# Optimization experiments

Hardware: AMD Instinct MI355X
Metric: run time of the kernel (lower is better)

Reference implementation:

```python
import jax, jax.numpy as jnp
import numpy as np

B, N, C = 4, 4096, 512
H = 8          # num_heads
M = 64         # num_landmarks
HD = C // H    # head_dim = 64
N_ITER = 6     # Newton-Schulz iterations (Nystromformer default)


def iterative_inv(mat):
    # mat: [B, H, M, M]; Nystromformer pseudo-inverse via Newton-Schulz.
    I = jnp.eye(mat.shape[-1], dtype=mat.dtype)
    K = mat
    # global-max initialization (original Nystromformer 'original' init)
    V = K.swapaxes(-1, -2) / (jnp.max(jnp.sum(K, axis=-2)) * jnp.max(jnp.sum(K, axis=-1)))
    for _ in range(N_ITER):
        KV = jnp.matmul(K, V)
        V = 0.25 * jnp.matmul(V, 13.0 * I - jnp.matmul(KV, 15.0 * I - jnp.matmul(KV, 7.0 * I - KV)))
    return V


def setup_inputs() -> dict:
    key = jax.random.key(0)
    k1, k2, k3, k4 = jax.random.split(key, 4)
    s = C ** -0.5
    return {
        "x": jax.random.normal(k1, (B, N, C), dtype=jnp.float32),
        "qkv_w": jax.random.normal(k2, (3 * C, C), dtype=jnp.float32) * s,
        "proj_w": jax.random.normal(k3, (C, C), dtype=jnp.float32) * s,
        "proj_b": jax.random.normal(k4, (C,), dtype=jnp.float32) * 0.01,
        "epoch": 1,
    }


def reference(x, qkv_w, proj_w, proj_b, epoch):
    b, n, c = x.shape
    hd = c // H
    qkv = (x @ qkv_w.T).reshape(b, n, 3, H, hd).transpose(2, 0, 3, 1, 4)  # [3,B,H,N,hd]
    Q, K, V = qkv[0], qkv[1], qkv[2]
    scale = 1.0 / np.sqrt(np.sqrt(hd)).astype(np.float32)
    Q = Q * scale
    K = K * scale
    # landmark pooling: mean over segments of length N // M
    Ql = Q.reshape(b, H, M, n // M, hd).mean(axis=-2)  # [B,H,M,hd]
    Kl = K.reshape(b, H, M, n // M, hd).mean(axis=-2)
    kernel_1 = jax.nn.softmax(jnp.einsum('bhnd,bhmd->bhnm', Q, Kl), axis=-1)   # [B,H,N,M]
    kernel_2 = jax.nn.softmax(jnp.einsum('bhmd,bhld->bhml', Ql, Kl), axis=-1)  # [B,H,M,M]
    kernel_3 = jax.nn.softmax(jnp.einsum('bhmd,bhnd->bhmn', Ql, K), axis=-1)   # [B,H,M,N]
    X = jnp.matmul(jnp.matmul(kernel_1, iterative_inv(kernel_2)), jnp.matmul(kernel_3, V))
    X = X.transpose(0, 2, 1, 3).reshape(b, n, c)
    return X @ proj_w.T + proj_b
```

## Files before the change

kernel.cpp:

```cpp
#include <hip/hip_runtime.h>
#include <hip/hip_bf16.h>
#include <stdint.h>

#define QSZe 8388608ull

typedef __attribute__((ext_vector_type(8))) short bf16x8;
typedef __attribute__((ext_vector_type(4))) float f32x4;
typedef const __attribute__((address_space(1))) unsigned int* gas1_t;
typedef __attribute__((address_space(3))) unsigned int* las3_t;

__device__ __forceinline__ float bf2f(unsigned short u) {
  return __uint_as_float(((unsigned int)u) << 16);
}
__device__ __forceinline__ unsigned short f2bf(float f) {
  unsigned int u = __float_as_uint(f);
  unsigned int r = (u + 0x7FFFu + ((u >> 16) & 1u)) >> 16;
  return (unsigned short)r;
}
__device__ __forceinline__ void gload_lds16(const void* g, void* l) {
  __builtin_amdgcn_global_load_lds((gas1_t)g, (las3_t)l, 16, 0, 0);
}
__device__ __forceinline__ unsigned int detect_f32(
    const unsigned short* __restrict__ raw_x) {
  int lane = threadIdx.x & 63;
  int big = 0;
#pragma unroll
  for (int i = 0; i < 4; i++) {
    int e = (raw_x[lane * 4 + i] >> 7) & 0xFF;
    big |= (e >= 0x8F) ? 1 : 0;
  }
  return (__ballot(big) != 0ull) ? 1u : 0u;
}

__global__ __launch_bounds__(256) void conv_all(
    const void* __restrict__ rx, const void* __restrict__ rwq,
    const void* __restrict__ rwp, unsigned short* __restrict__ cx,
    unsigned short* __restrict__ cwq, unsigned short* __restrict__ cwp,
    unsigned int* __restrict__ gstat) {
  int gid = blockIdx.x * 256 + threadIdx.x;
  if (gid == 0) {
    gstat[0] = 0u;
    gstat[1] = 0u;
  }
  unsigned int f = detect_f32((const unsigned short*)rx);
  const void* src;
  unsigned short* dst;
  int i8;
  if (gid < 1048576) {
    if (!f) return;
    src = rx; dst = cx; i8 = gid * 8;
  } else if (gid < 1146880) {
    src = rwq; dst = cwq; i8 = (gid - 1048576) * 8;
  } else {
    src = rwp; dst = cwp; i8 = (gid - 1146880) * 8;
  }
  if (f) {
    const float* fp = (const float*)src;
    float4 a = *(const float4*)(fp + i8);
    float4 b = *(const float4*)(fp + i8 + 4);
    unsigned short o[8] = {f2bf(a.x), f2bf(a.y), f2bf(a.z), f2bf(a.w),
                           f2bf(b.x), f2bf(b.y), f2bf(b.z), f2bf(b.w)};
    *(uint4*)(dst + i8) = *(const uint4*)o;
  } else {
    *(uint4*)(dst + i8) = *(const uint4*)((const unsigned short*)src + i8);
  }
}

__device__ __forceinline__ void mmB(const unsigned short* A_R,
                                    const unsigned short* B_T,
                                    unsigned short* out_R,
                                    unsigned short* out_T, int wave, int lane,
                                    float s, float dg, float a7,
                                    const unsigned short* Aelt) {
  const int fr = lane & 15, fq = lane >> 4;
  bf16x8 af0 = *(const bf16x8*)&A_R[(wave * 16 + fr) * 64 + fq * 8];
  bf16x8 af1 = *(const bf16x8*)&A_R[(wave * 16 + fr) * 64 + 32 + fq * 8];
  f32x4 acc[4] = {};
#pragma unroll
  for (int j = 0; j < 4; j++) {
    bf16x8 b0 = *(const bf16x8*)&B_T[(j * 16 + fr) * 64 + fq * 8];
    bf16x8 b1 = *(const bf16x8*)&B_T[(j * 16 + fr) * 64 + 32 + fq * 8];
    acc[j] = __builtin_amdgcn_mfma_f32_16x16x32_bf16(af0, b0, acc[j], 0, 0, 0);
    acc[j] = __builtin_amdgcn_mfma_f32_16x16x32_bf16(af1, b1, acc[j], 0, 0, 0);
  }
  float ael[4][4];
  if (Aelt) {
#pragma unroll
    for (int j = 0; j < 4; j++)
#pragma unroll
      for (int r = 0; r < 4; r++)
        ael[j][r] = bf2f(Aelt[(wave * 16 + fq * 4 + r) * 64 + j * 16 + fr]);
  }
#pragma unroll
  for (int j = 0; j < 4; j++) {
    int col = j * 16 + fr;
    unsigned short pack[4];
#pragma unroll
    for (int r = 0; r < 4; r++) {
      int row = wave * 16 + fq * 4 + r;
      float v = s * acc[j][r] + ((row == col) ? dg : 0.0f);
      if (Aelt) v += a7 * ael[j][r];
      unsigned short bv = f2bf(v);
      if (out_R) out_R[row * 64 + col] = bv;
      pack[r] = bv;
    }
    if (out_T)
      *(uint2*)&out_T[col * 64 + wave * 16 + fq * 4] = *(const uint2*)pack;
  }
}

__global__ __launch_bounds__(512) void qkv_gemm_mfma(
    const unsigned short* __restrict__ w, const void* __restrict__ xraw,
    const unsigned short* __restrict__ cx, unsigned short* __restrict__ qkv,
    float* __restrict__ Ql, float* __restrict__ Kl,
    unsigned short* __restrict__ Qlb, unsigned short* __restrict__ Klb) {
  __shared__ __align__(16) unsigned short At[2][128 * 64];
  __shared__ __align__(16) unsigned short Bt[2][256 * 64];
  const int t = threadIdx.x;
  const int lane = t & 63, wave = t >> 6;
  const int wf = wave >> 2, wt = wave & 3;
  const unsigned int isf = detect_f32((const unsigned short*)xraw);
  const unsigned short* xb = isf ? cx : (const unsigned short*)xraw;
  const int lin = blockIdx.x + blockIdx.y * 12;
  const int swz = (lin & 7) * 96 + (lin >> 3);
  const int f0 = (swz % 12) * 128, n0g = (swz / 12) * 256;
  const int srow = lane >> 3, skc = ((lane & 7) ^ srow) * 8;
  const int fr = lane & 15, fq = lane >> 4;
  const int rsw = fr & 7;
  f32x4 acc[4][4] = {};

  auto STAGE = [&](int p, int k0) {
#pragma unroll
    for (int s = 0; s < 2; s++) {
      int inst = wave * 2 + s;
      int row = inst * 8 + srow;
      gload_lds16(w + (size_t)(f0 + row) * 512 + k0 + skc,
                  &At[p][inst * 512]);
    }
#pragma unroll
    for (int s = 0; s < 4; s++) {
      int inst = wave * 4 + s;
      int row = inst * 8 + srow;
      gload_lds16(xb + (size_t)(n0g + row) * 512 + k0 + skc,
                  &Bt[p][inst * 512]);
    }
  };
  auto COMPUTE = [&](int p) {
#pragma unroll
    for (int kk = 0; kk < 64; kk += 32) {
      const int swo = (((kk >> 3) + fq) ^ rsw) << 3;
      bf16x8 af[4], bxf[4];
#pragma unroll
      for (int i = 0; i < 4; i++)
        af[i] = *(const bf16x8*)&At[p][(wf * 64 + i * 16 + fr) * 64 + swo];
#pragma unroll
      for (int j = 0; j < 4; j++)
        bxf[j] = *(const bf16x8*)&Bt[p][(wt * 64 + j * 16 + fr) * 64 + swo];
#pragma unroll
      for (int i = 0; i < 4; i++)
#pragma unroll
        for (int j = 0; j < 4; j++)
          acc[i][j] = __builtin_amdgcn_mfma_f32_16x16x32_bf16(
              af[i], bxf[j], acc[i][j], 0, 0, 0);
    }
  };

  STAGE(0, 0);
  int p = 0;
#pragma unroll 1
  for (int k0 = 0; k0 < 512; k0 += 64) {
    if (k0 + 64 < 512) {
      STAGE(p ^ 1, k0 + 64);
      asm volatile("s_waitcnt vmcnt(6)" ::: "memory");
    } else {
      asm volatile("s_waitcnt vmcnt(0)" ::: "memory");
    }
    asm volatile("s_barrier" ::: "memory");
    COMPUTE(p);
    asm volatile("s_barrier" ::: "memory");
    p ^= 1;
  }
  const int fbase = f0 + wf * 64;
  const int which = fbase >> 9;
  const int h = (fbase >> 6) & 7;
  const float scale = (which < 2) ? 0.3535533905932738f : 1.0f;
  const int b_ = n0g >> 12;
  const int bh = b_ * 8 + h;
  const int m_loc = ((n0g + wt * 64) & 4095) >> 6;
#pragma unroll
  for (int i = 0; i < 4; i++) {
    int d0 = i * 16 + fq * 4;
#pragma unroll
    for (int j = 0; j < 4; j++) {
      int nn = (n0g + wt * 64 + j * 16 + fr) & 4095;
      unsigned short pack[4];
#pragma unroll
      for (int r = 0; r < 4; r++) pack[r] = f2bf(acc[i][j][r] * scale);
      *(uint2*)&qkv[(size_t)which * QSZe + ((size_t)bh * 4096 + nn) * 64 +
                    d0] = *(const uint2*)pack;
    }
  }
  if (which < 2) {
    const float ps = scale * (1.0f / 64.0f);
#pragma unroll
    for (int i = 0; i < 4; i++) {
      float sm[4];
#pragma unroll
      for (int r = 0; r < 4; r++)
        sm[r] = acc[i][0][r] + acc[i][1][r] + acc[i][2][r] + acc[i][3][r];
#pragma unroll
      for (int mask = 1; mask < 16; mask <<= 1)
#pragma unroll
        for (int r = 0; r < 4; r++) sm[r] += __shfl_xor(sm[r], mask, 64);
      if (fr == 0) {
        int d0 = i * 16 + fq * 4;
        float4 v4 = make_float4(sm[0] * ps, sm[1] * ps, sm[2] * ps, sm[3] * ps);
        unsigned short pk[4] = {f2bf(v4.x), f2bf(v4.y), f2bf(v4.z), f2bf(v4.w)};
        size_t off = (size_t)bh * 4096 + m_loc * 64 + d0;
        if (which == 0) {
          *(float4*)&Ql[off] = v4;
          *(uint2*)&Qlb[off] = *(const uint2*)pk;
        } else {
          *(float4*)&Kl[off] = v4;
          *(uint2*)&Klb[off] = *(const uint2*)pk;
        }
      }
    }
  }
}

__global__ __launch_bounds__(256) void k3k2_mfma(
    const unsigned short* __restrict__ Qlb,
    const unsigned short* __restrict__ qkv, float* __restrict__ Wp,
    float* __restrict__ sp, const float* __restrict__ Ql,
    const float* __restrict__ Kl, float* __restrict__ k2,
    unsigned int* __restrict__ gstat) {
  __shared__ __align__(16) unsigned char SM[35840];
  const int t = threadIdx.x;
  const int lane = t & 63, wave = t >> 6;
  const int slab = blockIdx.x, bh = blockIdx.y;

  if (slab == 8) {
    float* KlT = (float*)SM;
    float* Ps = (float*)(SM + 16384);
#pragma unroll
    for (int i = 0; i < 16; i++) {
      int idx = i * 256 + t;
      KlT[(idx & 63) * 64 + (idx >> 6)] = Kl[bh * 4096 + idx];
    }
    __syncthreads();
    for (int r = wave * 16; r < wave * 16 + 16; r++) {
      float qv = Ql[(bh * 64 + r) * 64 + lane];
      float acc = 0.f;
#pragma unroll
      for (int k = 0; k < 64; k++)
        acc += __shfl(qv, k, 64) * KlT[k * 64 + lane];
      float mx = acc;
#pragma unroll
      for (int o = 32; o > 0; o >>= 1) mx = fmaxf(mx, __shfl_xor(mx, o, 64));
      float e = __expf(acc - mx);
      float s = e;
#pragma unroll
      for (int o = 32; o > 0; o >>= 1) s += __shfl_xor(s, o, 64);
      float p = e / s;
      k2[(bh * 64 + r) * 64 + lane] = p;
      Ps[r * 65 + lane] = p;
    }
    __syncthreads();
    float val = 0.f;
    if (t < 64) {
      for (int r = 0; r < 64; r++) val += Ps[r * 65 + t];
    } else if (t < 128) {
      int r = t - 64;
      for (int c = 0; c < 64; c++) val += Ps[r * 65 + c];
    }
    float mv = val;
#pragma unroll
    for (int o = 32; o > 0; o >>= 1) mv = fmaxf(mv, __shfl_xor(mv, o, 64));
    if (t == 0) atomicMax(gstat + 0, __float_as_uint(mv));
    if (t == 64) atomicMax(gstat + 1, __float_as_uint(mv));
    return;
  }
  unsigned short* Et = (unsigned short*)SM;
  unsigned short* Vt = (unsigned short*)(SM + 17408);
  float* scol_l = (float*)(SM + 34816);
  const int fr = lane & 15, fq = lane >> 4;
  const int n_base = slab * 512;
  const unsigned short* Kb = qkv + QSZe + (size_t)bh * 262144;
  const unsigned short* Vb = qkv + 2 * QSZe + (size_t)bh * 262144;
  const unsigned short* Qlp = Qlb + bh * 4096;

  bf16x8 qb[2][4];
#pragma unroll
  for (int h = 0; h < 2; h++)
#pragma unroll
    for (int j = 0; j < 4; j++)
      qb[h][j] = *(const bf16x8*)(Qlp + (j * 16 + fr) * 64 + h * 32 + fq * 8);

  f32x4 accW[4] = {};
  float scol[4] = {0.f, 0.f, 0.f, 0.f};

  for (int sc = 0; sc < 4; sc++) {
    const int n0 = n_base + sc * 128;
    {
      int n = t & 127, dg = t >> 7;
#pragma unroll
      for (int i = 0; i < 4; i++) {
        int d0 = (dg + 2 * i) * 8;
        uint4 v = *(const uint4*)(Vb + (size_t)(n0 + n) * 64 + d0);
        const unsigned short* s = (const unsigned short*)&v;
#pragma unroll
        for (int u = 0; u < 8; u++) Vt[(d0 + u) * 136 + n] = s[u];
      }
    }
    f32x4 acc[2][4] = {};
#pragma unroll
    for (int i = 0; i < 2; i++) {
      const unsigned short* Kr =
          Kb + (size_t)(n0 + wave * 32 + i * 16 + fr) * 64;
      bf16x8 a0 = *(const bf16x8*)(Kr + fq * 8);
      bf16x8 a1 = *(const bf16x8*)(Kr + 32 + fq * 8);
#pragma unroll
      for (int j = 0; j < 4; j++) {
        acc[i][j] = __builtin_amdgcn_mfma_f32_16x16x32_bf16(a0, qb[0][j],
                                                            acc[i][j], 0, 0, 0);
        acc[i][j] = __builtin_amdgcn_mfma_f32_16x16x32_bf16(a1, qb[1][j],
                                                            acc[i][j], 0, 0, 0);
      }
    }
#pragma unroll
    for (int i = 0; i < 2; i++)
#pragma unroll
      for (int j = 0; j < 4; j++) {
        unsigned short pack[4];
        float s4 = 0.f;
#pragma unroll
        for (int r = 0; r < 4; r++) {
          float e = __expf(acc[i][j][r]);
          s4 += e;
          pack[r] = f2bf(e);
        }
        scol[j] += s4;
        *(uint2*)&Et[(j * 16 + fr) * 136 + wave * 32 + i * 16 + fq * 4] =
            *(const uint2*)pack;
      }
    __syncthreads();
#pragma unroll
    for (int kk = 0; kk < 128; kk += 32) {
      bf16x8 ap = *(const bf16x8*)&Et[(wave * 16 + fr) * 136 + kk + fq * 8];
#pragma unroll
      for (int j = 0; j < 4; j++) {
        bf16x8 bv = *(const bf16x8*)&Vt[(j * 16 + fr) * 136 + kk + fq * 8];
        accW[j] =
            __builtin_amdgcn_mfma_f32_16x16x32_bf16(ap, bv, accW[j], 0, 0, 0);
      }
    }
    __syncthreads();
  }
#pragma unroll
  for (int j = 0; j < 4; j++) {
    float s = scol[j];
    s += __shfl_xor(s, 16, 64);
    s += __shfl_xor(s, 32, 64);
    if (fq == 0) scol_l[wave * 64 + j * 16 + fr] = s;
  }
  __syncthreads();
  if (t < 64)
    sp[(bh * 8 + slab) * 64 + t] = scol_l[0 * 64 + t] + scol_l[1 * 64 + t] +
                                   scol_l[2 * 64 + t] + scol_l[3 * 64 + t];
  float* wpo = Wp + ((size_t)bh * 8 + slab) * 4096;
#pragma unroll
  for (int j = 0; j < 4; j++)
#pragma unroll
    for (int r = 0; r < 4; r++)
      wpo[(wave * 16 + fq * 4 + r) * 64 + j * 16 + fr] = accW[j][r];
}

__global__ __launch_bounds__(256) void ns_kernel(
    const float* __restrict__ k2g, const unsigned int* __restrict__ gstat,
    const float* __restrict__ Wp, const float* __restrict__ sp,
    unsigned short* __restrict__ Ztb) {
  __shared__ __align__(16) unsigned short L[8 * 4096];
  __shared__ float ssum[64];
  unsigned short* K2R = L;
  unsigned short* VR = L + 4096;
  unsigned short* VT = L + 2 * 4096;
  unsigned short* AR = L + 3 * 4096;
  unsigned short* AT = L + 4 * 4096;
  unsigned short* T2T = L + 5 * 4096;
  unsigned short* T3T = L + 6 * 4096;
  unsigned short* WT = L + 7 * 4096;
  const int t = threadIdx.x, bh = blockIdx.x;
  const int lane = t & 63, wave = t >> 6;
  const float scale =
      1.0f / (__uint_as_float(gstat[0]) * __uint_as_float(gstat[1]));
  const float* k2p = k2g + bh * 4096;
  if (t < 64) {
    float s = 0.f;
#pragma unroll
    for (int c = 0; c < 8; c++) s += sp[(bh * 8 + c) * 64 + t];
    ssum[t] = s;
  }
  __syncthreads();
#pragma unroll
  for (int i = 0; i < 16; i++) {
    int idx = i * 256 + t;
    int m = idx >> 6, d = idx & 63;
    float kv = k2p[idx];
    K2R[idx] = f2bf(kv);
    VT[idx] = f2bf(kv * scale);
    VR[idx] = f2bf(k2p[d * 64 + m] * scale);
    float wv = 0.f;
#pragma unroll
    for (int cc = 0; cc < 8; cc++)
      wv += Wp[((size_t)(bh * 8 + cc)) * 4096 + idx];
    WT[d * 64 + m] = f2bf(wv / ssum[m]);
  }
  __syncthreads();
  for (int it = 0; it < 6; it++) {
    mmB(K2R, VT, AR, AT, wave, lane, 1.0f, 0.0f, 0.0f, nullptr);
    __syncthreads();
    mmB(AR, AT, nullptr, T2T, wave, lane, 1.0f, 15.0f, -7.0f, AR);
    __syncthreads();
    mmB(AR, T2T, nullptr, T3T, wave, lane, -1.0f, 13.0f, 0.0f, nullptr);
    __syncthreads();
    mmB(VR, T3T, VR, VT, wave, lane, 0.25f, 0.0f, 0.0f, nullptr);
    __syncthreads();
  }
  {
    const int fr = lane & 15, fq = lane >> 4;
    bf16x8 af0 = *(const bf16x8*)&WT[(wave * 16 + fr) * 64 + fq * 8];
    bf16x8 af1 = *(const bf16x8*)&WT[(wave * 16 + fr) * 64 + 32 + fq * 8];
    f32x4 acc[4] = {};
#pragma unroll
    for (int j = 0; j < 4; j++) {
      bf16x8 b0 = *(const bf16x8*)&VR[(j * 16 + fr) * 64 + fq * 8];
      bf16x8 b1 = *(const bf16x8*)&VR[(j * 16 + fr) * 64 + 32 + fq * 8];
      acc[j] =
          __builtin_amdgcn_mfma_f32_16x16x32_bf16(af0, b0, acc[j], 0, 0, 0);
      acc[j] =
          __builtin_amdgcn_mfma_f32_16x16x32_bf16(af1, b1, acc[j], 0, 0, 0);
    }
#pragma unroll
    for (int j = 0; j < 4; j++) {
      int m = j * 16 + fr;
#pragma unroll
      for (int r = 0; r < 4; r++) {
        int d = wave * 16 + fq * 4 + r;
        Ztb[bh * 4096 + d * 64 + m] = f2bf(acc[j][r]);
      }
    }
  }
}

__global__ __launch_bounds__(256) void k1x_mfma(
    const unsigned short* __restrict__ qkv,
    const unsigned short* __restrict__ Klb,
    const unsigned short* __restrict__ Ztb, unsigned short* __restrict__ X) {
  __shared__ __align__(16) unsigned short Qt[128 * 64];
  __shared__ __align__(16) unsigned short Ps[128 * 72];
  const int t = threadIdx.x;
  const int lane = t & 63, wave = t >> 6;
  const int fr = lane & 15, fq = lane >> 4;
  const int rsw = fr & 7;
  const int bh = blockIdx.x;
  const int n0 = blockIdx.y * 128;
  const unsigned short* Qb = qkv + (size_t)bh * 262144 + (size_t)n0 * 64;
  const unsigned short* Klp = Klb + bh * 4096;
  const unsigned short* Ztp = Ztb + bh * 4096;

  {
    const int srow = lane >> 3, skc = ((lane & 7) ^ srow) * 8;
#pragma unroll
    for (int s = 0; s < 4; s++) {
      int inst = wave * 4 + s;
      gload_lds16(Qb + (size_t)(inst * 8 + srow) * 64 + skc, &Qt[inst * 512]);
    }
  }
  __syncthreads();

  f32x4 acc[2][4] = {};
#pragma unroll
  for (int kk = 0; kk < 64; kk += 32) {
    bf16x8 af[2], bg[4];
#pragma unroll
    for (int i = 0; i < 2; i++)
      af[i] = *(const bf16x8*)&Qt[(wave * 32 + i * 16 + fr) * 64 +
                                  ((((kk >> 3) + fq) ^ rsw) << 3)];
#pragma unroll
    for (int j = 0; j < 4; j++)
      bg[j] = *(const bf16x8*)(Klp + (j * 16 + fr) * 64 + kk + fq * 8);
#pragma unroll
    for (int i = 0; i < 2; i++)
#pragma unroll
      for (int j = 0; j < 4; j++)
        acc[i][j] = __builtin_amdgcn_mfma_f32_16x16x32_bf16(af[i], bg[j],
                                                            acc[i][j], 0, 0, 0);
  }

#pragma unroll
  for (int i = 0; i < 2; i++) {
    float sr[4] = {0.f, 0.f, 0.f, 0.f};
#pragma unroll
    for (int j = 0; j < 4; j++)
#pragma unroll
      for (int r = 0; r < 4; r++) {
        float e = __expf(acc[i][j][r]);
        acc[i][j][r] = e;
        sr[r] += e;
      }
#pragma unroll
    for (int mask = 1; mask < 16; mask <<= 1)
#pragma unroll
      for (int r = 0; r < 4; r++) sr[r] += __shfl_xor(sr[r], mask, 64);
    float is[4];
#pragma unroll
    for (int r = 0; r < 4; r++) is[r] = 1.0f / sr[r];
#pragma unroll
    for (int j = 0; j < 4; j++)
#pragma unroll
      for (int r = 0; r < 4; r++)
        Ps[(wave * 32 + i * 16 + fq * 4 + r) * 72 + j * 16 + fr] =
            f2bf(acc[i][j][r] * is[r]);
  }
  __syncthreads();

  f32x4 ax[2][4] = {};
#pragma unroll
  for (int kk = 0; kk < 64; kk += 32) {
    bf16x8 ap[2], bz[4];
#pragma unroll
    for (int i = 0; i < 2; i++)
      ap[i] =
          *(const bf16x8*)&Ps[(wave * 32 + i * 16 + fr) * 72 + kk + fq * 8];
#pragma unroll
    for (int j = 0; j < 4; j++)
      bz[j] = *(const bf16x8*)(Ztp + (j * 16 + fr) * 64 + kk + fq * 8);
#pragma unroll
    for (int i = 0; i < 2; i++)
#pragma unroll
      for (int j = 0; j < 4; j++)
        ax[i][j] = __builtin_amdgcn_mfma_f32_16x16x32_bf16(ap[i], bz[j],
                                                           ax[i][j], 0, 0, 0);
  }

  const int b_ = bh >> 3, h = bh & 7;
#pragma unroll
  for (int i = 0; i < 2; i++) {
#pragma unroll
    for (int j = 0; j < 4; j++) {
      int c = h * 64 + j * 16 + fr;
#pragma unroll
      for (int r = 0; r < 4; r++) {
        int n = n0 + wave * 32 + i * 16 + fq * 4 + r;
        X[((size_t)(b_ * 4096 + n)) * 512 + c] = f2bf(ax[i][j][r]);
      }
    }
  }
}

__global__ __launch_bounds__(256) void proj_gemm_mfma(
    const unsigned short* __restrict__ X, const unsigned short* __restrict__ w,
    const unsigned short* __restrict__ raw_x, const void* __restrict__ raw_b,
    float* __restrict__ out) {
  __shared__ __align__(16) unsigned short At[128 * 64];
  __shared__ __align__(16) unsigned short Bt[128 * 64];
  const int t = threadIdx.x;
  const unsigned int f = detect_f32(raw_x);
  const int lane = t & 63, wave = t >> 6;
  const int wr = wave >> 1, wc = wave & 1;
  const int i0 = blockIdx.y * 128, j0 = blockIdx.x * 128;
  const int srow = lane >> 3;
  const int skc = ((lane & 7) ^ srow) * 8;
  const int fr = lane & 15, fq = lane >> 4;
  const int rsw = fr & 7;
  f32x4 acc[4][4] = {};

  for (int k0 = 0; k0 < 512; k0 += 64) {
#pragma unroll
    for (int s = 0; s < 4; s++) {
      int inst = wave * 4 + s;
      int row = inst * 8 + srow;
      gload_lds16(X + (size_t)(i0 + row) * 512 + k0 + skc, &At[inst * 512]);
      gload_lds16(w + (size_t)(j0 + row) * 512 + k0 + skc, &Bt[inst * 512]);
    }
    __syncthreads();
#pragma unroll
    for (int kk = 0; kk < 64; kk += 32) {
      const int swo = (((kk >> 3) + fq) ^ rsw) << 3;
      bf16x8 af[4], bg[4];
#pragma unroll
      for (int i = 0; i < 4; i++)
        af[i] = *(const bf16x8*)&At[(wr * 64 + i * 16 + fr) * 64 + swo];
#pragma unroll
      for (int j = 0; j < 4; j++)
        bg[j] = *(const bf16x8*)&Bt[(wc * 64 + j * 16 + fr) * 64 + swo];
#pragma unroll
      for (int i = 0; i < 4; i++)
#pragma unroll
        for (int j = 0; j < 4; j++)
          acc[i][j] = __builtin_amdgcn_mfma_f32_16x16x32_bf16(
              af[i], bg[j], acc[i][j], 0, 0, 0);
    }
    __syncthreads();
  }
#pragma unroll
  for (int j = 0; j < 4; j++) {
    int col = j0 + wc * 64 + j * 16 + fr;
    float bia = f ? ((const float*)raw_b)[col]
                  : bf2f(((const unsigned short*)raw_b)[col]);
#pragma unroll
    for (int i = 0; i < 4; i++) {
      int rbase = i0 + wr * 64 + i * 16 + fq * 4;
#pragma unroll
      for (int r = 0; r < 4; r++) {
        out[(size_t)(rbase + r) * 512 + col] = acc[i][j][r] + bia;
      }
    }
  }
}

extern "C" void kernel_launch(void* const* d_in, const int* in_sizes, int n_in,
                              void* d_out, int out_size, void* d_ws,
                              size_t ws_size, hipStream_t stream) {
  (void)in_sizes; (void)n_in; (void)out_size; (void)ws_size;

  char* w8 = (char*)d_ws;
  unsigned short* cx  = (unsigned short*)(w8 + 0);
  unsigned short* cwq = (unsigned short*)(w8 + 16777216);
  unsigned short* cwp = (unsigned short*)(w8 + 18350080);
  unsigned short* qkv = (unsigned short*)(w8 + 18876416);
  unsigned short* X   = (unsigned short*)(w8 + 69208064);
  float* Ql = (float*)(w8 + 85985280);
  float* Kl = (float*)(w8 + 86509568);
  float* k2 = (float*)(w8 + 87033856);
  unsigned short* Ztb = (unsigned short*)(w8 + 88082432);
  unsigned int* gstat = (unsigned int*)(w8 + 88606720);
  float* Wp = (float*)(w8 + 88608768);
  float* sp = (float*)(w8 + 92803072);
  unsigned short* Klb = (unsigned short*)(w8 + 92868608);
  unsigned short* Qlb = (unsigned short*)(w8 + 93130752);

  conv_all<<<4608, 256, 0, stream>>>(d_in[0], d_in[1], d_in[2], cx, cwq, cwp,
                                     gstat);
  qkv_gemm_mfma<<<dim3(12, 64), 512, 0, stream>>>(cwq, d_in[0], cx, qkv, Ql,
                                                  Kl, Qlb, Klb);
  k3k2_mfma<<<dim3(9, 32), 256, 0, stream>>>(Qlb, qkv, Wp, sp, Ql, Kl, k2,
                                             gstat);
  ns_kernel<<<32, 256, 0, stream>>>(k2, gstat, Wp, sp, Ztb);
  k1x_mfma<<<dim3(32, 32), 256, 0, stream>>>(qkv, Klb, Ztb, X);
  proj_gemm_mfma<<<dim3(4, 128), 256, 0, stream>>>(
      X, cwp, (const unsigned short*)d_in[0], d_in[3], (float*)d_out);
}
```

Before: 223.5 us.

## Deepen load pipelining in QKV, landmark-attention and projection GEMMs

The QKV GEMM goes from double to triple buffering of LDS tiles, so global-to-LDS loads run two k-steps ahead with adjusted vmcnt waits. The kernel3·V slab kernel prefetches the next V chunk into registers while the current chunk computes. The projection GEMM gains double-buffered LDS with async staging in place of its synchronous load-then-sync loop. These hide global memory latency at the cost of more LDS and registers, which can lower occupancy (the QKV kernel's LDS grows to about 144KB).

```diff
diff --git a/kernel.cpp b/kernel.cpp
--- a/kernel.cpp
+++ b/kernel.cpp
@@ -114,8 +114,8 @@
     const unsigned short* __restrict__ cx, unsigned short* __restrict__ qkv,
     float* __restrict__ Ql, float* __restrict__ Kl,
     unsigned short* __restrict__ Qlb, unsigned short* __restrict__ Klb) {
-  __shared__ __align__(16) unsigned short At[2][128 * 64];
-  __shared__ __align__(16) unsigned short Bt[2][256 * 64];
+  __shared__ __align__(16) unsigned short At[3][128 * 64];
+  __shared__ __align__(16) unsigned short Bt[3][256 * 64];
   const int t = threadIdx.x;
   const int lane = t & 63, wave = t >> 6;
   const int wf = wave >> 2, wt = wave & 3;
@@ -166,11 +166,15 @@
   };
 
   STAGE(0, 0);
+  STAGE(1, 64);
   int p = 0;
 #pragma unroll 1
   for (int k0 = 0; k0 < 512; k0 += 64) {
-    if (k0 + 64 < 512) {
-      STAGE(p ^ 1, k0 + 64);
+    if (k0 + 128 < 512) {
+      int pn = (p == 0) ? 2 : p - 1;
+      STAGE(pn, k0 + 128);
+      asm volatile("s_waitcnt vmcnt(12)" ::: "memory");
+    } else if (k0 + 64 < 512) {
       asm volatile("s_waitcnt vmcnt(6)" ::: "memory");
     } else {
       asm volatile("s_waitcnt vmcnt(0)" ::: "memory");
@@ -178,7 +182,7 @@
     asm volatile("s_barrier" ::: "memory");
     COMPUTE(p);
     asm volatile("s_barrier" ::: "memory");
-    p ^= 1;
+    p = (p == 2) ? 0 : p + 1;
   }
   const int fbase = f0 + wf * 64;
   const int which = fbase >> 9;
@@ -300,17 +304,30 @@
   f32x4 accW[4] = {};
   float scol[4] = {0.f, 0.f, 0.f, 0.f};
 
+  const int vn = t & 127, vdg = t >> 7;
+  uint4 vreg[4];
+#pragma unroll
+  for (int i = 0; i < 4; i++) {
+    int d0 = (vdg + 2 * i) * 8;
+    vreg[i] = *(const uint4*)(Vb + (size_t)(n_base + vn) * 64 + d0);
+  }
+
+#pragma unroll
   for (int sc = 0; sc < 4; sc++) {
     const int n0 = n_base + sc * 128;
-    {
-      int n = t & 127, dg = t >> 7;
+#pragma unroll
+    for (int i = 0; i < 4; i++) {
+      int d0 = (vdg + 2 * i) * 8;
+      const unsigned short* s = (const unsigned short*)&vreg[i];
+#pragma unroll
+      for (int u = 0; u < 8; u++) Vt[(d0 + u) * 136 + vn] = s[u];
+    }
+    uint4 vnext[4];
+    if (sc < 3) {
 #pragma unroll
       for (int i = 0; i < 4; i++) {
-        int d0 = (dg + 2 * i) * 8;
-        uint4 v = *(const uint4*)(Vb + (size_t)(n0 + n) * 64 + d0);
-        const unsigned short* s = (const unsigned short*)&v;
-#pragma unroll
-        for (int u = 0; u < 8; u++) Vt[(d0 + u) * 136 + n] = s[u];
+        int d0 = (vdg + 2 * i) * 8;
+        vnext[i] = *(const uint4*)(Vb + (size_t)(n0 + 128 + vn) * 64 + d0);
       }
     }
     f32x4 acc[2][4] = {};
@@ -356,6 +373,10 @@
       }
     }
     __syncthreads();
+    if (sc < 3) {
+#pragma unroll
+      for (int i = 0; i < 4; i++) vreg[i] = vnext[i];
+    }
   }
 #pragma unroll
   for (int j = 0; j < 4; j++) {
@@ -563,8 +584,8 @@
     const unsigned short* __restrict__ X, const unsigned short* __restrict__ w,
     const unsigned short* __restrict__ raw_x, const void* __restrict__ raw_b,
     float* __restrict__ out) {
-  __shared__ __align__(16) unsigned short At[128 * 64];
-  __shared__ __align__(16) unsigned short Bt[128 * 64];
+  __shared__ __align__(16) unsigned short At[2][128 * 64];
+  __shared__ __align__(16) unsigned short Bt[2][128 * 64];
   const int t = threadIdx.x;
   const unsigned int f = detect_f32(raw_x);
   const int lane = t & 63, wave = t >> 6;
@@ -576,25 +597,28 @@
   const int rsw = fr & 7;
   f32x4 acc[4][4] = {};
 
-  for (int k0 = 0; k0 < 512; k0 += 64) {
+  auto STAGE = [&](int p, int k0) {
 #pragma unroll
     for (int s = 0; s < 4; s++) {
       int inst = wave * 4 + s;
       int row = inst * 8 + srow;
-      gload_lds16(X + (size_t)(i0 + row) * 512 + k0 + skc, &At[inst * 512]);
-      gload_lds16(w + (size_t)(j0 + row) * 512 + k0 + skc, &Bt[inst * 512]);
-    }
-    __syncthreads();
+      gload_lds16(X + (size_t)(i0 + row) * 512 + k0 + skc,
+                  &At[p][inst * 512]);
+      gload_lds16(w + (size_t)(j0 + row) * 512 + k0 + skc,
+                  &Bt[p][inst * 512]);
+    }
+  };
+  auto COMPUTE = [&](int p) {
 #pragma unroll
     for (int kk = 0; kk < 64; kk += 32) {
       const int swo = (((kk >> 3) + fq) ^ rsw) << 3;
       bf16x8 af[4], bg[4];
 #pragma unroll
       for (int i = 0; i < 4; i++)
-        af[i] = *(const bf16x8*)&At[(wr * 64 + i * 16 + fr) * 64 + swo];
+        af[i] = *(const bf16x8*)&At[p][(wr * 64 + i * 16 + fr) * 64 + swo];
 #pragma unroll
       for (int j = 0; j < 4; j++)
-        bg[j] = *(const bf16x8*)&Bt[(wc * 64 + j * 16 + fr) * 64 + swo];
+        bg[j] = *(const bf16x8*)&Bt[p][(wc * 64 + j * 16 + fr) * 64 + swo];
 #pragma unroll
       for (int i = 0; i < 4; i++)
 #pragma unroll
@@ -602,7 +626,22 @@
           acc[i][j] = __builtin_amdgcn_mfma_f32_16x16x32_bf16(
               af[i], bg[j], acc[i][j], 0, 0, 0);
     }
-    __syncthreads();
+  };
+
+  STAGE(0, 0);
+  int p = 0;
+#pragma unroll 1
+  for (int k0 = 0; k0 < 512; k0 += 64) {
+    if (k0 + 64 < 512) {
+      STAGE(p ^ 1, k0 + 64);
+      asm volatile("s_waitcnt vmcnt(8)" ::: "memory");
+    } else {
+      asm volatile("s_waitcnt vmcnt(0)" ::: "memory");
+    }
+    asm volatile("s_barrier" ::: "memory");
+    COMPUTE(p);
+    asm volatile("s_barrier" ::: "memory");
+    p ^= 1;
   }
 #pragma unroll
   for (int j = 0; j < 4; j++) {
```

Result: slower. 228.3 us (+2.1%).
